# Performance work log

Measured on AMD Instinct MI355X. Metric: run time of the kernel, lower is better.

## Reference

```python
import jax, jax.numpy as jnp
import numpy as np

BETA = 0.25
K = 1024  # num_embeddings


def setup_inputs() -> dict:
    key = jax.random.key(0)
    k1, k2 = jax.random.split(key)
    x = jax.random.normal(k1, (32, 64, 64, 64), dtype=jnp.float32)  # [B, D, H, W]
    # nn.Embedding init: uniform(-1/K, 1/K)
    codebook = jax.random.uniform(k2, (K, 64), dtype=jnp.float32,
                                  minval=-1.0 / K, maxval=1.0 / K)
    return {"x": x, "codebook": codebook}


def reference(x, codebook):
    B, D, H, W = x.shape
    xp = jnp.transpose(x, (0, 2, 3, 1))            # [B, H, W, D]
    xf = xp.reshape(-1, D)                          # [N, D]
    # squared euclidean distances; argmin is identical to argmin of cdist
    d2 = (jnp.sum(xf * xf, axis=1, keepdims=True)
          - 2.0 * (xf @ codebook.T)
          + jnp.sum(codebook * codebook, axis=1))   # [N, K]
    idx = jnp.argmin(d2, axis=1)                    # [N]
    x_q = codebook[idx].reshape(xp.shape)           # [B, H, W, D]
    # training loss: codebook term + beta * commitment term
    loss = (jnp.mean((jax.lax.stop_gradient(x_q) - xp) ** 2)
            + BETA * jnp.mean((x_q - jax.lax.stop_gradient(xp)) ** 2))
    # straight-through estimator
    x_st = xp + jax.lax.stop_gradient(x_q - xp)
    out = jnp.transpose(x_st, (0, 3, 1, 2))         # [B, D, H, W]
    return out, loss
```

## Files before the change

### kernel.cpp

```cpp
#include <hip/hip_runtime.h>
#include <cfloat>


#define DD   64
#define HHWW 4096
#define KC   1024
#define NBLK  2048
#define NPOSD 8388608.0f

typedef __bf16  bf16x8 __attribute__((ext_vector_type(8)));
typedef float   f32x4  __attribute__((ext_vector_type(4)));

__device__ __forceinline__ unsigned short bf16_bits(float f) {
  unsigned u = __float_as_uint(f);
  return (unsigned short)((u + 0x7FFFu + ((u >> 16) & 1u)) >> 16);
}

__device__ __forceinline__ unsigned int umax2(unsigned int a, unsigned int b) {
  return a > b ? a : b;
}

__global__ __launch_bounds__(256) void vq_pre(
    const float* __restrict__ cb,
    unsigned short* __restrict__ cb_frag,
    float* __restrict__ hneg4)
{
  const int gt = blockIdx.x * 256 + threadIdx.x;
  const int k  = gt >> 4;
  const int q  = gt & 15;
  const float4 v = *(const float4*)(cb + (size_t)k * DD + q * 4);

  float s = v.x * v.x + v.y * v.y + v.z * v.z + v.w * v.w;
#pragma unroll
  for (int m = 1; m < 16; m <<= 1) s += __shfl_xor(s, m, 64);
  if (q == 0) {
    const float mval = 1.0f - 0.5f * s;
    float4 m4; m4.x = mval; m4.y = mval; m4.z = mval; m4.w = mval;
    *(float4*)(hneg4 + (size_t)k * 4) = m4;
  }

  const int d0 = q * 4;
  const int kk = d0 >> 5, g = (d0 >> 3) & 3, e0 = d0 & 7;
  const int t = k >> 4, l15 = k & 15;
  unsigned short u0 = bf16_bits(v.x), u1 = bf16_bits(v.y);
  unsigned short u2 = bf16_bits(v.z), u3 = bf16_bits(v.w);
  uint2 wv2;
  wv2.x = (unsigned int)u0 | ((unsigned int)u1 << 16);
  wv2.y = (unsigned int)u2 | ((unsigned int)u3 << 16);
  *(uint2*)(&cb_frag[(((t * 2 + kk) * 64) + (g * 16 + l15)) * 8 + e0]) = wv2;
}

__global__ __launch_bounds__(256) void vq_main(
    const float* __restrict__ x,
    const unsigned short* __restrict__ cb_frag,
    const float* __restrict__ hneg4,
    const float* __restrict__ cb,
    float* __restrict__ out,
    float* __restrict__ partials)
{
  __shared__ unsigned short xfrag[4096];
  __shared__ unsigned int   cand[2][64];
  __shared__ int            idx_lds[64];
  __shared__ float          xred[4];

  const int tid  = threadIdx.x;
  const int wv   = tid >> 6;
  const int lane = tid & 63;
  const int l15  = lane & 15;
  const int cw   = wv & 1;
  const int pw   = wv >> 1;

  const int row = ((blockIdx.x & 7) << 8) + (blockIdx.x >> 3);
  const int b   = row >> 6;
  const int h   = row & 63;
  const float* xb = x + (size_t)b * DD * HHWW + h * 64;

  float xacc = 0.f;
#pragma unroll
  for (int r4 = 0; r4 < 4; ++r4) {
    const int m  = tid + r4 * 256;
    const int d  = m >> 4;
    const int w4 = m & 15;
    const float4 v4 = *(const float4*)(xb + (size_t)d * HHWW + w4 * 4);
    const int kk = d >> 5, gg = (d >> 3) & 3, e = d & 7;
    const int pt = w4 >> 2;
    const int base = pt * 1024 + kk * 512 + gg * 128 + e;
    const int lb = (w4 & 3) * 4;
    xacc += v4.x * v4.x + v4.y * v4.y + v4.z * v4.z + v4.w * v4.w;
    xfrag[base + ((lb + 0) ^ pt) * 8] = bf16_bits(v4.x);
    xfrag[base + ((lb + 1) ^ pt) * 8] = bf16_bits(v4.y);
    xfrag[base + ((lb + 2) ^ pt) * 8] = bf16_bits(v4.z);
    xfrag[base + ((lb + 3) ^ pt) * 8] = bf16_bits(v4.w);
  }

  __syncthreads();

  const int g = lane >> 4;
  bf16x8 afrag[2][2];
#pragma unroll
  for (int j = 0; j < 2; ++j) {
    const int pt = pw * 2 + j;
    const int ls = g * 16 + (l15 ^ pt);
    afrag[j][0] = *(const bf16x8*)(&xfrag[pt * 1024 + ls * 8]);
    afrag[j][1] = *(const bf16x8*)(&xfrag[pt * 1024 + 512 + ls * 8]);
  }

  unsigned int best[2][4];
#pragma unroll
  for (int j = 0; j < 2; ++j)
#pragma unroll
    for (int rr = 0; rr < 4; ++rr) best[j][rr] = 0u;

  const unsigned int MASK = 0xFFFFFC00u;
  const int codec0 = 1023 - cw * 512 - l15;
  const char*  bb  = (const char*)cb_frag + (size_t)cw * 32 * 2048 + (size_t)lane * 16;
  const f32x4* mhp = (const f32x4*)hneg4 + cw * 512 + l15;

  bf16x8 pb0[2], pb1[2];
  f32x4  pmh[2];
#pragma unroll
  for (int s = 0; s < 2; ++s) {
    pb0[s] = *(const bf16x8*)(bb + s * 2048);
    pb1[s] = *(const bf16x8*)(bb + s * 2048 + 1024);
    pmh[s] = mhp[s * 16];
  }

#pragma unroll 4
  for (int t = 0; t < 32; ++t) {
    const int s = t & 1;
    const bf16x8 b0 = pb0[s], b1 = pb1[s];
    const f32x4  mh = pmh[s];
    const int tn = (t + 2) & 31;
    pb0[s] = *(const bf16x8*)(bb + tn * 2048);
    pb1[s] = *(const bf16x8*)(bb + tn * 2048 + 1024);
    pmh[s] = mhp[tn * 16];

    const unsigned int codec = (unsigned int)(codec0 - t * 16);

#pragma unroll
    for (int j = 0; j < 2; ++j) {
      f32x4 acc = __builtin_amdgcn_mfma_f32_16x16x32_bf16(afrag[j][0], b0, mh, 0, 0, 0);
      acc = __builtin_amdgcn_mfma_f32_16x16x32_bf16(afrag[j][1], b1, acc, 0, 0, 0);
#pragma unroll
      for (int rr = 0; rr < 4; ++rr) {
        const unsigned int p = (__float_as_uint(acc[rr]) & MASK) | codec;
        best[j][rr] = umax2(best[j][rr], p);
      }
    }
  }

#pragma unroll
  for (int j = 0; j < 2; ++j)
#pragma unroll
    for (int rr = 0; rr < 4; ++rr) {
      unsigned int v = best[j][rr];
#pragma unroll
      for (int m = 1; m < 16; m <<= 1) {
        unsigned int vo = __shfl_xor(v, m, 64);
        v = umax2(v, vo);
      }
      if (l15 == 0) cand[cw][pw * 32 + j * 16 + g * 4 + rr] = v;
    }

#pragma unroll
  for (int m = 1; m < 64; m <<= 1) xacc += __shfl_xor(xacc, m, 64);
  if (lane == 0) xred[wv] = xacc;

  __syncthreads();

  if (tid < 64) {
    const unsigned int v = umax2(cand[0][tid], cand[1][tid]);
    idx_lds[tid] = 1023 - (int)(v & 1023u);
    float vt1 = __uint_as_float(v & MASK) - 1.0f;
#pragma unroll
    for (int m = 1; m < 64; m <<= 1) vt1 += __shfl_xor(vt1, m, 64);
    if (tid == 0)
      partials[blockIdx.x] =
          (xred[0] + xred[1] + xred[2] + xred[3]) - 2.0f * vt1;
  }

  __syncthreads();

  const int myidx = idx_lds[lane];
  const float4* crow = (const float4*)(cb + (size_t)myidx * DD) + wv * 4;
  const float4 c0 = crow[0], c1 = crow[1], c2 = crow[2], c3 = crow[3];
  float* ob = out + (size_t)b * DD * HHWW + h * 64 + lane;
  ob[(size_t)(wv * 16 +  0) * HHWW] = c0.x;
  ob[(size_t)(wv * 16 +  1) * HHWW] = c0.y;
  ob[(size_t)(wv * 16 +  2) * HHWW] = c0.z;
  ob[(size_t)(wv * 16 +  3) * HHWW] = c0.w;
  ob[(size_t)(wv * 16 +  4) * HHWW] = c1.x;
  ob[(size_t)(wv * 16 +  5) * HHWW] = c1.y;
  ob[(size_t)(wv * 16 +  6) * HHWW] = c1.z;
  ob[(size_t)(wv * 16 +  7) * HHWW] = c1.w;
  ob[(size_t)(wv * 16 +  8) * HHWW] = c2.x;
  ob[(size_t)(wv * 16 +  9) * HHWW] = c2.y;
  ob[(size_t)(wv * 16 + 10) * HHWW] = c2.z;
  ob[(size_t)(wv * 16 + 11) * HHWW] = c2.w;
  ob[(size_t)(wv * 16 + 12) * HHWW] = c3.x;
  ob[(size_t)(wv * 16 + 13) * HHWW] = c3.y;
  ob[(size_t)(wv * 16 + 14) * HHWW] = c3.z;
  ob[(size_t)(wv * 16 + 15) * HHWW] = c3.w;
}

__global__ __launch_bounds__(256) void vq_loss(
    const float* __restrict__ partials, float* __restrict__ loss_out)
{
  __shared__ float sred[4];
  int tid = threadIdx.x;
  float s = 0.f;
  for (int i = tid; i < NBLK; i += 256) s += partials[i];
#pragma unroll
  for (int m = 1; m < 64; m <<= 1) s += __shfl_xor(s, m, 64);
  if ((tid & 63) == 0) sred[tid >> 6] = s;
  __syncthreads();
  if (tid == 0)
    loss_out[0] = (sred[0] + sred[1] + sred[2] + sred[3]) * (1.25f / NPOSD);
}

extern "C" void kernel_launch(void* const* d_in, const int* in_sizes, int n_in,
                              void* d_out, int out_size, void* d_ws, size_t ws_size,
                              hipStream_t stream) {
  const float* x  = (const float*)d_in[0];
  const float* cb = (const float*)d_in[1];
  float* out      = (float*)d_out;
  float* loss_out = out + 8388608;

  char* ws = (char*)d_ws;
  unsigned short* cb_frag = (unsigned short*)(ws);
  float* hneg4    = (float*)(ws + 131072);
  float* partials = (float*)(ws + 147456);

  vq_pre <<<64,   256, 0, stream>>>(cb, cb_frag, hneg4);
  vq_main<<<NBLK, 256, 0, stream>>>(x, cb_frag, hneg4, cb, out, partials);
  vq_loss<<<1,    256, 0, stream>>>(partials, loss_out);
}
```

Baseline: 48.76 us.

## Stage codebook in LDS via async global_load_lds and process two rows per block

After: 46.71 us. 4.2% less time.

```diff
diff --git a/kernel.cpp b/kernel.cpp
--- a/kernel.cpp
+++ b/kernel.cpp
@@ -2,10 +2,10 @@
 #include <cfloat>
 
 
-#define DD   64
-#define HHWW 4096
-#define KC   1024
-#define NBLK  2048
+#define DD    64
+#define HHWW  4096
+#define KC    1024
+#define NBLKM 1024
 #define NPOSD 8388608.0f
 
 typedef __bf16  bf16x8 __attribute__((ext_vector_type(8)));
@@ -18,6 +18,12 @@
 
 __device__ __forceinline__ unsigned int umax2(unsigned int a, unsigned int b) {
   return a > b ? a : b;
+}
+
+__device__ __forceinline__ void gload_lds16(const void* gsrc, void* ldst) {
+  __builtin_amdgcn_global_load_lds(
+      (const __attribute__((address_space(1))) unsigned int*)gsrc,
+      (__attribute__((address_space(3))) unsigned int*)ldst, 16, 0, 0);
 }
 
 __global__ __launch_bounds__(256) void vq_pre(
@@ -58,51 +64,64 @@
     float* __restrict__ out,
     float* __restrict__ partials)
 {
-  __shared__ unsigned short xfrag[4096];
-  __shared__ unsigned int   cand[2][64];
-  __shared__ int            idx_lds[64];
+  __shared__ unsigned short cbbuf[2][8192];
+  __shared__ unsigned short xfrag[2][4096];
+  __shared__ int            idx_lds[2][64];
   __shared__ float          xred[4];
+  __shared__ float          vtred[4];
 
   const int tid  = threadIdx.x;
   const int wv   = tid >> 6;
   const int lane = tid & 63;
   const int l15  = lane & 15;
-  const int cw   = wv & 1;
-  const int pw   = wv >> 1;
-
-  const int row = ((blockIdx.x & 7) << 8) + (blockIdx.x >> 3);
-  const int b   = row >> 6;
-  const int h   = row & 63;
-  const float* xb = x + (size_t)b * DD * HHWW + h * 64;
+  const int g    = lane >> 4;
+  const int rw   = wv >> 1;
+  const int phf  = wv & 1;
+
+  const int row0 = (((blockIdx.x & 7) << 7) + (blockIdx.x >> 3)) * 2;
+  const int b    = row0 >> 6;
+  const int h0   = row0 & 63;
+  const float* xb = x + (size_t)b * DD * HHWW + h0 * 64;
+
+#pragma unroll
+  for (int i = 0; i < 4; ++i)
+    gload_lds16((const char*)cb_frag + i * 4096 + (size_t)tid * 16,
+                (char*)cbbuf[0] + i * 4096 + wv * 1024);
 
   float xacc = 0.f;
 #pragma unroll
-  for (int r4 = 0; r4 < 4; ++r4) {
-    const int m  = tid + r4 * 256;
-    const int d  = m >> 4;
-    const int w4 = m & 15;
-    const float4 v4 = *(const float4*)(xb + (size_t)d * HHWW + w4 * 4);
-    const int kk = d >> 5, gg = (d >> 3) & 3, e = d & 7;
-    const int pt = w4 >> 2;
-    const int base = pt * 1024 + kk * 512 + gg * 128 + e;
-    const int lb = (w4 & 3) * 4;
-    xacc += v4.x * v4.x + v4.y * v4.y + v4.z * v4.z + v4.w * v4.w;
-    xfrag[base + ((lb + 0) ^ pt) * 8] = bf16_bits(v4.x);
-    xfrag[base + ((lb + 1) ^ pt) * 8] = bf16_bits(v4.y);
-    xfrag[base + ((lb + 2) ^ pt) * 8] = bf16_bits(v4.z);
-    xfrag[base + ((lb + 3) ^ pt) * 8] = bf16_bits(v4.w);
-  }
+  for (int r = 0; r < 2; ++r) {
+#pragma unroll
+    for (int r4 = 0; r4 < 4; ++r4) {
+      const int m  = tid + r4 * 256;
+      const int d  = m >> 4;
+      const int w4 = m & 15;
+      const float4 v4 = *(const float4*)(xb + (size_t)d * HHWW + r * 64 + w4 * 4);
+      const int kk = d >> 5, gg = (d >> 3) & 3, e = d & 7;
+      const int pt = w4 >> 2;
+      const int base = pt * 1024 + kk * 512 + gg * 128 + e;
+      const int lb = (w4 & 3) * 4;
+      xacc += v4.x * v4.x + v4.y * v4.y + v4.z * v4.z + v4.w * v4.w;
+      xfrag[r][base + ((lb + 0) ^ pt) * 8] = bf16_bits(v4.x);
+      xfrag[r][base + ((lb + 1) ^ pt) * 8] = bf16_bits(v4.y);
+      xfrag[r][base + ((lb + 2) ^ pt) * 8] = bf16_bits(v4.z);
+      xfrag[r][base + ((lb + 3) ^ pt) * 8] = bf16_bits(v4.w);
+    }
+  }
+
+  const f32x4* mhp = (const f32x4*)hneg4 + l15;
+  f32x4 nmhA = mhp[0];
+  f32x4 nmhB = mhp[16];
 
   __syncthreads();
 
-  const int g = lane >> 4;
   bf16x8 afrag[2][2];
 #pragma unroll
   for (int j = 0; j < 2; ++j) {
-    const int pt = pw * 2 + j;
+    const int pt = phf * 2 + j;
     const int ls = g * 16 + (l15 ^ pt);
-    afrag[j][0] = *(const bf16x8*)(&xfrag[pt * 1024 + ls * 8]);
-    afrag[j][1] = *(const bf16x8*)(&xfrag[pt * 1024 + 512 + ls * 8]);
+    afrag[j][0] = *(const bf16x8*)(&xfrag[rw][pt * 1024 + ls * 8]);
+    afrag[j][1] = *(const bf16x8*)(&xfrag[rw][pt * 1024 + 512 + ls * 8]);
   }
 
   unsigned int best[2][4];
@@ -112,43 +131,50 @@
     for (int rr = 0; rr < 4; ++rr) best[j][rr] = 0u;
 
   const unsigned int MASK = 0xFFFFFC00u;
-  const int codec0 = 1023 - cw * 512 - l15;
-  const char*  bb  = (const char*)cb_frag + (size_t)cw * 32 * 2048 + (size_t)lane * 16;
-  const f32x4* mhp = (const f32x4*)hneg4 + cw * 512 + l15;
-
-  bf16x8 pb0[2], pb1[2];
-  f32x4  pmh[2];
-#pragma unroll
-  for (int s = 0; s < 2; ++s) {
-    pb0[s] = *(const bf16x8*)(bb + s * 2048);
-    pb1[s] = *(const bf16x8*)(bb + s * 2048 + 1024);
-    pmh[s] = mhp[s * 16];
-  }
-
-#pragma unroll 4
-  for (int t = 0; t < 32; ++t) {
-    const int s = t & 1;
-    const bf16x8 b0 = pb0[s], b1 = pb1[s];
-    const f32x4  mh = pmh[s];
-    const int tn = (t + 2) & 31;
-    pb0[s] = *(const bf16x8*)(bb + tn * 2048);
-    pb1[s] = *(const bf16x8*)(bb + tn * 2048 + 1024);
-    pmh[s] = mhp[tn * 16];
-
-    const unsigned int codec = (unsigned int)(codec0 - t * 16);
-
-#pragma unroll
-    for (int j = 0; j < 2; ++j) {
-      f32x4 acc = __builtin_amdgcn_mfma_f32_16x16x32_bf16(afrag[j][0], b0, mh, 0, 0, 0);
-      acc = __builtin_amdgcn_mfma_f32_16x16x32_bf16(afrag[j][1], b1, acc, 0, 0, 0);
-#pragma unroll
-      for (int rr = 0; rr < 4; ++rr) {
-        const unsigned int p = (__float_as_uint(acc[rr]) & MASK) | codec;
-        best[j][rr] = umax2(best[j][rr], p);
+  const int codec0 = 1023 - l15;
+
+  for (int ph = 0; ph < 8; ++ph) {
+    if (ph < 7) {
+#pragma unroll
+      for (int i = 0; i < 4; ++i)
+        gload_lds16((const char*)cb_frag + (ph + 1) * 16384 + i * 4096 + (size_t)tid * 16,
+                    (char*)cbbuf[(ph + 1) & 1] + i * 4096 + wv * 1024);
+    }
+
+    const unsigned short* bufc = cbbuf[ph & 1];
+#pragma unroll
+    for (int pr = 0; pr < 4; ++pr) {
+      const int tA = ph * 8 + pr * 2;
+      const bf16x8 bA0 = *(const bf16x8*)(bufc + pr * 2048 + lane * 8);
+      const bf16x8 bA1 = *(const bf16x8*)(bufc + pr * 2048 + 512 + lane * 8);
+      const bf16x8 bB0 = *(const bf16x8*)(bufc + pr * 2048 + 1024 + lane * 8);
+      const bf16x8 bB1 = *(const bf16x8*)(bufc + pr * 2048 + 1536 + lane * 8);
+      const f32x4 mhA = nmhA, mhB = nmhB;
+      const int tn = (tA + 2) & 63;
+      nmhA = mhp[tn * 16];
+      nmhB = mhp[(tn + 1) * 16];
+
+      const unsigned int codecA = (unsigned int)(codec0 - tA * 16);
+      const unsigned int codecB = (unsigned int)(codec0 - (tA + 1) * 16);
+
+#pragma unroll
+      for (int j = 0; j < 2; ++j) {
+        f32x4 aA = __builtin_amdgcn_mfma_f32_16x16x32_bf16(afrag[j][0], bA0, mhA, 0, 0, 0);
+        aA = __builtin_amdgcn_mfma_f32_16x16x32_bf16(afrag[j][1], bA1, aA, 0, 0, 0);
+        f32x4 aB = __builtin_amdgcn_mfma_f32_16x16x32_bf16(afrag[j][0], bB0, mhB, 0, 0, 0);
+        aB = __builtin_amdgcn_mfma_f32_16x16x32_bf16(afrag[j][1], bB1, aB, 0, 0, 0);
+#pragma unroll
+        for (int rr = 0; rr < 4; ++rr) {
+          const unsigned int pA_ = (__float_as_uint(aA[rr]) & MASK) | codecA;
+          const unsigned int pB_ = (__float_as_uint(aB[rr]) & MASK) | codecB;
+          best[j][rr] = umax2(umax2(best[j][rr], pA_), pB_);
+        }
       }
     }
-  }
-
+    __syncthreads();
+  }
+
+  float vtacc = 0.f;
 #pragma unroll
   for (int j = 0; j < 2; ++j)
 #pragma unroll
@@ -159,48 +185,49 @@
         unsigned int vo = __shfl_xor(v, m, 64);
         v = umax2(v, vo);
       }
-      if (l15 == 0) cand[cw][pw * 32 + j * 16 + g * 4 + rr] = v;
-    }
-
-#pragma unroll
-  for (int m = 1; m < 64; m <<= 1) xacc += __shfl_xor(xacc, m, 64);
-  if (lane == 0) xred[wv] = xacc;
+      if (l15 == 0) {
+        idx_lds[rw][(phf * 2 + j) * 16 + g * 4 + rr] = 1023 - (int)(v & 1023u);
+        vtacc += __uint_as_float(v & MASK) - 1.0f;
+      }
+    }
+
+#pragma unroll
+  for (int m = 1; m < 64; m <<= 1) {
+    xacc  += __shfl_xor(xacc, m, 64);
+    vtacc += __shfl_xor(vtacc, m, 64);
+  }
+  if (lane == 0) { xred[wv] = xacc; vtred[wv] = vtacc; }
 
   __syncthreads();
 
-  if (tid < 64) {
-    const unsigned int v = umax2(cand[0][tid], cand[1][tid]);
-    idx_lds[tid] = 1023 - (int)(v & 1023u);
-    float vt1 = __uint_as_float(v & MASK) - 1.0f;
-#pragma unroll
-    for (int m = 1; m < 64; m <<= 1) vt1 += __shfl_xor(vt1, m, 64);
-    if (tid == 0)
-      partials[blockIdx.x] =
-          (xred[0] + xred[1] + xred[2] + xred[3]) - 2.0f * vt1;
-  }
-
-  __syncthreads();
-
-  const int myidx = idx_lds[lane];
-  const float4* crow = (const float4*)(cb + (size_t)myidx * DD) + wv * 4;
-  const float4 c0 = crow[0], c1 = crow[1], c2 = crow[2], c3 = crow[3];
-  float* ob = out + (size_t)b * DD * HHWW + h * 64 + lane;
-  ob[(size_t)(wv * 16 +  0) * HHWW] = c0.x;
-  ob[(size_t)(wv * 16 +  1) * HHWW] = c0.y;
-  ob[(size_t)(wv * 16 +  2) * HHWW] = c0.z;
-  ob[(size_t)(wv * 16 +  3) * HHWW] = c0.w;
-  ob[(size_t)(wv * 16 +  4) * HHWW] = c1.x;
-  ob[(size_t)(wv * 16 +  5) * HHWW] = c1.y;
-  ob[(size_t)(wv * 16 +  6) * HHWW] = c1.z;
-  ob[(size_t)(wv * 16 +  7) * HHWW] = c1.w;
-  ob[(size_t)(wv * 16 +  8) * HHWW] = c2.x;
-  ob[(size_t)(wv * 16 +  9) * HHWW] = c2.y;
-  ob[(size_t)(wv * 16 + 10) * HHWW] = c2.z;
-  ob[(size_t)(wv * 16 + 11) * HHWW] = c2.w;
-  ob[(size_t)(wv * 16 + 12) * HHWW] = c3.x;
-  ob[(size_t)(wv * 16 + 13) * HHWW] = c3.y;
-  ob[(size_t)(wv * 16 + 14) * HHWW] = c3.z;
-  ob[(size_t)(wv * 16 + 15) * HHWW] = c3.w;
+  if (tid == 0)
+    partials[blockIdx.x] =
+        (xred[0] + xred[1] + xred[2] + xred[3]) -
+        2.0f * (vtred[0] + vtred[1] + vtred[2] + vtred[3]);
+
+#pragma unroll
+  for (int r = 0; r < 2; ++r) {
+    const int myidx = idx_lds[r][lane];
+    const float4* crow = (const float4*)(cb + (size_t)myidx * DD) + wv * 4;
+    const float4 c0 = crow[0], c1 = crow[1], c2 = crow[2], c3 = crow[3];
+    float* ob = out + (size_t)b * DD * HHWW + (h0 + r) * 64 + lane;
+    ob[(size_t)(wv * 16 +  0) * HHWW] = c0.x;
+    ob[(size_t)(wv * 16 +  1) * HHWW] = c0.y;
+    ob[(size_t)(wv * 16 +  2) * HHWW] = c0.z;
+    ob[(size_t)(wv * 16 +  3) * HHWW] = c0.w;
+    ob[(size_t)(wv * 16 +  4) * HHWW] = c1.x;
+    ob[(size_t)(wv * 16 +  5) * HHWW] = c1.y;
+    ob[(size_t)(wv * 16 +  6) * HHWW] = c1.z;
+    ob[(size_t)(wv * 16 +  7) * HHWW] = c1.w;
+    ob[(size_t)(wv * 16 +  8) * HHWW] = c2.x;
+    ob[(size_t)(wv * 16 +  9) * HHWW] = c2.y;
+    ob[(size_t)(wv * 16 + 10) * HHWW] = c2.z;
+    ob[(size_t)(wv * 16 + 11) * HHWW] = c2.w;
+    ob[(size_t)(wv * 16 + 12) * HHWW] = c3.x;
+    ob[(size_t)(wv * 16 + 13) * HHWW] = c3.y;
+    ob[(size_t)(wv * 16 + 14) * HHWW] = c3.z;
+    ob[(size_t)(wv * 16 + 15) * HHWW] = c3.w;
+  }
 }
 
 __global__ __launch_bounds__(256) void vq_loss(
@@ -209,7 +236,7 @@
   __shared__ float sred[4];
   int tid = threadIdx.x;
   float s = 0.f;
-  for (int i = tid; i < NBLK; i += 256) s += partials[i];
+  for (int i = tid; i < NBLKM; i += 256) s += partials[i];
 #pragma unroll
   for (int m = 1; m < 64; m <<= 1) s += __shfl_xor(s, m, 64);
   if ((tid & 63) == 0) sred[tid >> 6] = s;
@@ -231,7 +258,7 @@
   float* hneg4    = (float*)(ws + 131072);
   float* partials = (float*)(ws + 147456);
 
-  vq_pre <<<64,   256, 0, stream>>>(cb, cb_frag, hneg4);
-  vq_main<<<NBLK, 256, 0, stream>>>(x, cb_frag, hneg4, cb, out, partials);
-  vq_loss<<<1,    256, 0, stream>>>(partials, loss_out);
-}
+  vq_pre <<<64,    256, 0, stream>>>(cb, cb_frag, hneg4);
+  vq_main<<<NBLKM, 256, 0, stream>>>(x, cb_frag, hneg4, cb, out, partials);
+  vq_loss<<<1,     256, 0, stream>>>(partials, loss_out);
+}
```
